# Kernel tuning notes

Hardware: AMD Instinct MI355X
Metric: run time of the kernel (lower is better)

The kernel has to match this reference:

```python
import jax, jax.numpy as jnp
import numpy as np

THRESHOLD = 0.5
TEMPERATURE = 4.0
LOG_CLAMP = -100.0  # torch BCELoss clamps log terms at -100

B, C, K = 131072, 128, 64


def setup_inputs() -> dict:
    key = jax.random.key(0)
    k1, k2, k3, k4, k5 = jax.random.split(key, 5)
    # sigmoid-like probabilities in (0, 1)
    output = jax.random.uniform(k1, (B, C), dtype=jnp.float32)
    output_consistency = jax.random.uniform(k2, (B, C), dtype=jnp.float32)
    label = jax.random.uniform(k3, (B, C), dtype=jnp.float32)
    class_idx = jnp.sort(jax.random.randint(k4, (K,), 0, C)).astype(jnp.int64)
    batch_mask = jax.random.randint(k5, (B,), 0, 2).astype(bool)
    return {
        "output": output,
        "output_consistency": output_consistency,
        "label": label,
        "class_idx": class_idx,
        "batch_mask": batch_mask,
    }


def _clamped_log(x):
    return jnp.maximum(jnp.log(x), LOG_CLAMP)


def reference(output, output_consistency, label, class_idx, batch_mask):
    # gather the class columns of interest: [B, K]
    o = output[:, class_idx]
    oc = output_consistency[:, class_idx]
    y = label[:, class_idx]

    # sharpened pseudo-label (branch on threshold, fused via where)
    sharp = jnp.where(o > THRESHOLD,
                      o + (1.0 - o) / TEMPERATURE,
                      o - o / TEMPERATURE)

    # per-element BCE (torch BCELoss semantics with log clamp)
    bce = -(y * _clamped_log(o) + (1.0 - y) * _clamped_log(1.0 - o))
    pseudo = (o - sharp) ** 2          # F.mse_loss on scalars
    consistency = (oc - sharp) ** 2

    per_elem = bce + pseudo + consistency            # [B, K]
    row_mask = batch_mask.astype(per_elem.dtype)     # [B]
    total = jnp.sum(per_elem * row_mask[:, None])
    cnt = jnp.sum(row_mask) * per_elem.shape[1]
    return total / cnt
```

## Files before the change

kernel.cpp:

```cpp
#include <hip/hip_runtime.h>

#define BLOCK   256
#define B_ROWS  131072
#define C_COLS  128
#define K_SEL   64
#define ROWS_PER_BLOCK 64
#define GRID    (B_ROWS / ROWS_PER_BLOCK)
#define F4_PER_BLOCK (ROWS_PER_BLOCK * C_COLS / 4)
#define ITERS   (F4_PER_BLOCK / BLOCK)

#define WS_PARTIALS_OFF 1024

__global__ void build_w(const int* __restrict__ class_idx,
                        float* __restrict__ w)
{
    int c = threadIdx.x;
    int cnt = 0;
    #pragma unroll
    for (int k = 0; k < K_SEL; ++k)
        cnt += (class_idx[k] == c) ? 1 : 0;
    w[c] = (float)cnt;
}

__device__ __forceinline__ float fast_log(float x) {
    return __log2f(x) * 0.6931471805599453f;
}

__device__ __forceinline__ float per_elem_loss(float o, float oc, float y,
                                               float wc) {
    float sharp = (o > 0.5f) ? (o + (1.0f - o) * 0.25f)
                             : (o - o * 0.25f);
    float lo  = fmaxf(fast_log(o),        -100.0f);
    float l1o = fmaxf(fast_log(1.0f - o), -100.0f);
    float bce = -(y * lo + (1.0f - y) * l1o);
    float dp = o  - sharp;
    float dc = oc - sharp;
    return wc * (bce + dp * dp + dc * dc);
}

__global__ __launch_bounds__(BLOCK) void semi_loss_main(
    const float* __restrict__ out,
    const float* __restrict__ outc,
    const float* __restrict__ lab,
    const int*  __restrict__ batch_mask,
    const float* __restrict__ wtab,
    float2* __restrict__ partials)
{
    __shared__ float wm[ROWS_PER_BLOCK];

    const int row0 = blockIdx.x * ROWS_PER_BLOCK;
    float cntf = 0.0f;
    if (threadIdx.x < ROWS_PER_BLOCK) {
        float m = batch_mask[row0 + threadIdx.x] ? 1.0f : 0.0f;
        wm[threadIdx.x] = m;
        cntf = m;
    }

    const int   c4 = threadIdx.x & 31;
    const float4 w4 = ((const float4*)wtab)[c4];

    __syncthreads();

    const int vbase = blockIdx.x * F4_PER_BLOCK + threadIdx.x;
    const int rsub  = threadIdx.x >> 5;
    float sum = 0.0f;

    #pragma unroll
    for (int i = 0; i < ITERS; ++i) {
        const float m = wm[i * 8 + rsub];
        if (m > 0.0f) {
            const int v = vbase + i * BLOCK;
            float4 o4  = ((const float4*)out )[v];
            float4 oc4 = ((const float4*)outc)[v];
            float4 y4  = ((const float4*)lab )[v];
            sum += per_elem_loss(o4.x, oc4.x, y4.x, w4.x)
                 + per_elem_loss(o4.y, oc4.y, y4.y, w4.y)
                 + per_elem_loss(o4.z, oc4.z, y4.z, w4.z)
                 + per_elem_loss(o4.w, oc4.w, y4.w, w4.w);
        }
    }

    #pragma unroll
    for (int off = 32; off > 0; off >>= 1) {
        sum  += __shfl_down(sum,  off);
        cntf += __shfl_down(cntf, off);
    }
    __shared__ float ssum[BLOCK / 64];
    __shared__ float scnt[BLOCK / 64];
    int wave = threadIdx.x >> 6;
    int lane = threadIdx.x & 63;
    if (lane == 0) { ssum[wave] = sum; scnt[wave] = cntf; }
    __syncthreads();
    if (threadIdx.x == 0) {
        float s = 0.0f, c = 0.0f;
        #pragma unroll
        for (int i = 0; i < BLOCK / 64; ++i) { s += ssum[i]; c += scnt[i]; }
        partials[blockIdx.x] = make_float2(s, c);
    }
}

__global__ __launch_bounds__(BLOCK) void semi_loss_reduce(
    const float2* __restrict__ partials, float* __restrict__ out)
{
    double s = 0.0, c = 0.0;
    for (int i = threadIdx.x; i < GRID; i += BLOCK) {
        float2 p = partials[i];
        s += (double)p.x;
        c += (double)p.y;
    }
    #pragma unroll
    for (int off = 32; off > 0; off >>= 1) {
        s += __shfl_down(s, off);
        c += __shfl_down(c, off);
    }
    __shared__ double dsum[BLOCK / 64];
    __shared__ double dcnt[BLOCK / 64];
    int wave = threadIdx.x >> 6;
    int lane = threadIdx.x & 63;
    if (lane == 0) { dsum[wave] = s; dcnt[wave] = c; }
    __syncthreads();
    if (threadIdx.x == 0) {
        double ts = 0.0, tc = 0.0;
        #pragma unroll
        for (int i = 0; i < BLOCK / 64; ++i) { ts += dsum[i]; tc += dcnt[i]; }
        out[0] = (float)(ts / (tc * (double)K_SEL));
    }
}

extern "C" void kernel_launch(void* const* d_in, const int* in_sizes, int n_in,
                              void* d_out, int out_size, void* d_ws, size_t ws_size,
                              hipStream_t stream) {
    const float* out_p  = (const float*)d_in[0];
    const float* outc_p = (const float*)d_in[1];
    const float* lab_p  = (const float*)d_in[2];
    const int*   cidx_p = (const int*)d_in[3];
    const int*   mask_p = (const int*)d_in[4];

    float*  wtab     = (float*)d_ws;
    float2* partials = (float2*)((char*)d_ws + WS_PARTIALS_OFF);

    build_w<<<1, C_COLS, 0, stream>>>(cidx_p, wtab);
    semi_loss_main<<<GRID, BLOCK, 0, stream>>>(out_p, outc_p, lab_p,
                                               mask_p, wtab, partials);
    semi_loss_reduce<<<1, BLOCK, 0, stream>>>(partials, (float*)d_out);
}
```

Measured before the change: 186.5 us.

## Compact active rows via ballot/atomic and process only masked-in rows

Adds a stream-compaction pass that writes the indices of rows with batch_mask set into a workspace list using wave ballots and an atomic counter. The main kernel then launches over the compacted list and loads all rows up front with no per-row branch, so every wave works on active rows and exits early once past the active count. The row count now comes from the atomic counter instead of a per-block partial. This adds an extra kernel launch plus the compaction read/write, and makes row ordering nondeterministic, which can change float summation order.

After: 210.9 us. 1.13x slower.

```diff
diff --git a/kernel.cpp b/kernel.cpp
--- a/kernel.cpp
+++ b/kernel.cpp
@@ -1,25 +1,48 @@
 #include <hip/hip_runtime.h>
 
-#define BLOCK   256
-#define B_ROWS  131072
-#define C_COLS  128
-#define K_SEL   64
-#define ROWS_PER_BLOCK 64
-#define GRID    (B_ROWS / ROWS_PER_BLOCK)
-#define F4_PER_BLOCK (ROWS_PER_BLOCK * C_COLS / 4)
-#define ITERS   (F4_PER_BLOCK / BLOCK)
+#define BLOCK    256
+#define B_ROWS   131072
+#define C_COLS   128
+#define K_SEL    64
+#define F4_PER_ROW (C_COLS / 4)
 
+#define ROWS_PB   32
+#define GRID_MAIN (B_ROWS / ROWS_PB)
+
+#define GRID_CMP  (B_ROWS / BLOCK)
+
+#define WS_COUNT_OFF    512
 #define WS_PARTIALS_OFF 1024
+#define WS_ROWIDS_OFF   65536
 
-__global__ void build_w(const int* __restrict__ class_idx,
-                        float* __restrict__ w)
+__global__ void init_count(int* count) { *count = 0; }
+
+__global__ void compact_and_w(const int* __restrict__ batch_mask,
+                              const int* __restrict__ class_idx,
+                              int* __restrict__ count,
+                              int* __restrict__ rowids,
+                              float* __restrict__ w)
 {
-    int c = threadIdx.x;
-    int cnt = 0;
-    #pragma unroll
-    for (int k = 0; k < K_SEL; ++k)
-        cnt += (class_idx[k] == c) ? 1 : 0;
-    w[c] = (float)cnt;
+    if (blockIdx.x == GRID_CMP) {
+        if (threadIdx.x < C_COLS) {
+            int c = threadIdx.x, cnt = 0;
+            #pragma unroll
+            for (int k = 0; k < K_SEL; ++k)
+                cnt += (class_idx[k] == c) ? 1 : 0;
+            w[c] = (float)cnt;
+        }
+        return;
+    }
+    const int row = blockIdx.x * BLOCK + threadIdx.x;
+    const int m   = batch_mask[row] ? 1 : 0;
+    const unsigned long long b = __ballot(m);
+    const int lane   = threadIdx.x & 63;
+    const int wcount = __popcll(b);
+    const int prefix = __popcll(b & ((1ULL << lane) - 1ULL));
+    int base = 0;
+    if (lane == 0 && wcount) base = atomicAdd(count, wcount);
+    base = __shfl(base, 0);
+    if (m) rowids[base + prefix] = row;
 }
 
 __device__ __forceinline__ float fast_log(float x) {
@@ -38,92 +61,102 @@
     return wc * (bce + dp * dp + dc * dc);
 }
 
-__global__ __launch_bounds__(BLOCK) void semi_loss_main(
+__global__ __launch_bounds__(BLOCK, 4) void semi_loss_main(
     const float* __restrict__ out,
     const float* __restrict__ outc,
     const float* __restrict__ lab,
-    const int*  __restrict__ batch_mask,
+    const int*  __restrict__ count,
+    const int*  __restrict__ rowids,
     const float* __restrict__ wtab,
-    float2* __restrict__ partials)
+    float* __restrict__ partials)
 {
-    __shared__ float wm[ROWS_PER_BLOCK];
+    const int nact = *count;
+    const int base = blockIdx.x * ROWS_PB;
 
-    const int row0 = blockIdx.x * ROWS_PER_BLOCK;
-    float cntf = 0.0f;
-    if (threadIdx.x < ROWS_PER_BLOCK) {
-        float m = batch_mask[row0 + threadIdx.x] ? 1.0f : 0.0f;
-        wm[threadIdx.x] = m;
-        cntf = m;
+    if (base >= nact) {
+        if (threadIdx.x == 0) partials[blockIdx.x] = 0.0f;
+        return;
     }
 
-    const int   c4 = threadIdx.x & 31;
-    const float4 w4 = ((const float4*)wtab)[c4];
-
+    __shared__ int   srow[ROWS_PB];
+    __shared__ float sval[ROWS_PB];
+    if (threadIdx.x < ROWS_PB) {
+        int idx = base + threadIdx.x;
+        srow[threadIdx.x] = (idx < nact) ? rowids[idx] : rowids[base];
+        sval[threadIdx.x] = (idx < nact) ? 1.0f : 0.0f;
+    }
+    const int cq = threadIdx.x & 31;
+    const float4 w4 = ((const float4*)wtab)[cq];
     __syncthreads();
 
-    const int vbase = blockIdx.x * F4_PER_BLOCK + threadIdx.x;
-    const int rsub  = threadIdx.x >> 5;
+    const int lr0 = threadIdx.x >> 5;
+
+    int   v[4];
+    float val[4];
+    #pragma unroll
+    for (int i = 0; i < 4; ++i) {
+        int lr = lr0 + 8 * i;
+        v[i]   = srow[lr] * F4_PER_ROW + cq;
+        val[i] = sval[lr];
+    }
+
+    float4 o4[4], oc4[4], y4[4];
+    #pragma unroll
+    for (int i = 0; i < 4; ++i) {
+        o4[i]  = ((const float4*)out )[v[i]];
+        oc4[i] = ((const float4*)outc)[v[i]];
+        y4[i]  = ((const float4*)lab )[v[i]];
+    }
+
     float sum = 0.0f;
-
     #pragma unroll
-    for (int i = 0; i < ITERS; ++i) {
-        const float m = wm[i * 8 + rsub];
-        if (m > 0.0f) {
-            const int v = vbase + i * BLOCK;
-            float4 o4  = ((const float4*)out )[v];
-            float4 oc4 = ((const float4*)outc)[v];
-            float4 y4  = ((const float4*)lab )[v];
-            sum += per_elem_loss(o4.x, oc4.x, y4.x, w4.x)
-                 + per_elem_loss(o4.y, oc4.y, y4.y, w4.y)
-                 + per_elem_loss(o4.z, oc4.z, y4.z, w4.z)
-                 + per_elem_loss(o4.w, oc4.w, y4.w, w4.w);
-        }
+    for (int i = 0; i < 4; ++i) {
+        float s = per_elem_loss(o4[i].x, oc4[i].x, y4[i].x, w4.x)
+                + per_elem_loss(o4[i].y, oc4[i].y, y4[i].y, w4.y)
+                + per_elem_loss(o4[i].z, oc4[i].z, y4[i].z, w4.z)
+                + per_elem_loss(o4[i].w, oc4[i].w, y4[i].w, w4.w);
+        sum += val[i] * s;
     }
 
     #pragma unroll
-    for (int off = 32; off > 0; off >>= 1) {
-        sum  += __shfl_down(sum,  off);
-        cntf += __shfl_down(cntf, off);
-    }
+    for (int off = 32; off > 0; off >>= 1)
+        sum += __shfl_down(sum, off);
+
     __shared__ float ssum[BLOCK / 64];
-    __shared__ float scnt[BLOCK / 64];
     int wave = threadIdx.x >> 6;
     int lane = threadIdx.x & 63;
-    if (lane == 0) { ssum[wave] = sum; scnt[wave] = cntf; }
+    if (lane == 0) ssum[wave] = sum;
     __syncthreads();
     if (threadIdx.x == 0) {
-        float s = 0.0f, c = 0.0f;
+        float s = 0.0f;
         #pragma unroll
-        for (int i = 0; i < BLOCK / 64; ++i) { s += ssum[i]; c += scnt[i]; }
-        partials[blockIdx.x] = make_float2(s, c);
+        for (int i = 0; i < BLOCK / 64; ++i) s += ssum[i];
+        partials[blockIdx.x] = s;
     }
 }
 
 __global__ __launch_bounds__(BLOCK) void semi_loss_reduce(
-    const float2* __restrict__ partials, float* __restrict__ out)
+    const float* __restrict__ partials,
+    const int*  __restrict__ count,
+    float* __restrict__ outv)
 {
-    double s = 0.0, c = 0.0;
-    for (int i = threadIdx.x; i < GRID; i += BLOCK) {
-        float2 p = partials[i];
-        s += (double)p.x;
-        c += (double)p.y;
-    }
+    double s = 0.0;
+    for (int i = threadIdx.x; i < GRID_MAIN; i += BLOCK)
+        s += (double)partials[i];
     #pragma unroll
-    for (int off = 32; off > 0; off >>= 1) {
+    for (int off = 32; off > 0; off >>= 1)
         s += __shfl_down(s, off);
-        c += __shfl_down(c, off);
-    }
     __shared__ double dsum[BLOCK / 64];
-    __shared__ double dcnt[BLOCK / 64];
     int wave = threadIdx.x >> 6;
     int lane = threadIdx.x & 63;
-    if (lane == 0) { dsum[wave] = s; dcnt[wave] = c; }
+    if (lane == 0) dsum[wave] = s;
     __syncthreads();
     if (threadIdx.x == 0) {
-        double ts = 0.0, tc = 0.0;
+        double ts = 0.0;
         #pragma unroll
-        for (int i = 0; i < BLOCK / 64; ++i) { ts += dsum[i]; tc += dcnt[i]; }
-        out[0] = (float)(ts / (tc * (double)K_SEL));
+        for (int i = 0; i < BLOCK / 64; ++i) ts += dsum[i];
+        int n = *count;
+        outv[0] = (n > 0) ? (float)(ts / ((double)n * (double)K_SEL)) : 0.0f;
     }
 }
 
@@ -136,11 +169,16 @@
     const int*   cidx_p = (const int*)d_in[3];
     const int*   mask_p = (const int*)d_in[4];
 
-    float*  wtab     = (float*)d_ws;
-    float2* partials = (float2*)((char*)d_ws + WS_PARTIALS_OFF);
+    float* wtab     = (float*)d_ws;
+    int*   count    = (int*)((char*)d_ws + WS_COUNT_OFF);
+    float* partials = (float*)((char*)d_ws + WS_PARTIALS_OFF);
+    int*   rowids   = (int*)((char*)d_ws + WS_ROWIDS_OFF);
 
-    build_w<<<1, C_COLS, 0, stream>>>(cidx_p, wtab);
-    semi_loss_main<<<GRID, BLOCK, 0, stream>>>(out_p, outc_p, lab_p,
-                                               mask_p, wtab, partials);
-    semi_loss_reduce<<<1, BLOCK, 0, stream>>>(partials, (float*)d_out);
+    init_count<<<1, 1, 0, stream>>>(count);
+    compact_and_w<<<GRID_CMP + 1, BLOCK, 0, stream>>>(mask_p, cidx_p,
+                                                      count, rowids, wtab);
+    semi_loss_main<<<GRID_MAIN, BLOCK, 0, stream>>>(out_p, outc_p, lab_p,
+                                                    count, rowids, wtab,
+                                                    partials);
+    semi_loss_reduce<<<1, BLOCK, 0, stream>>>(partials, count, (float*)d_out);
 }
```
